# Performance work log

Measured on AMD Instinct MI355X. Metric: run time of the kernel, lower is better.

The kernel has to match this reference:

```python
import jax, jax.numpy as jnp
import numpy as np

N, K, D = 65536, 4096, 256
COMMITMENT_COST = 0.25


def setup_inputs() -> dict:
    key = jax.random.key(0)
    k1, k2 = jax.random.split(key)
    z_flat = jax.random.normal(k1, (N, D), dtype=jnp.float32)
    # init_method='normal': std=0.02
    codebook = jax.random.normal(k2, (K, D), dtype=jnp.float32) * 0.02
    return {"z_flat": z_flat, "codebook": codebook}


def reference(z_flat, codebook):
    # distances[n,k] = ||z_n||^2 + ||e_k||^2 - 2 z_n . e_k   (squared L2)
    z_sq = jnp.sum(z_flat ** 2, axis=1, keepdims=True)            # [N,1]
    e_sq = jnp.sum(codebook ** 2, axis=1)                          # [K]
    distances = z_sq + e_sq - 2.0 * jnp.matmul(z_flat, codebook.T)  # [N,K]
    indices = jnp.argmin(distances, axis=1)                        # [N] int
    quantized = codebook[indices]                                  # [N,D]

    e_latent_loss = jnp.mean((jax.lax.stop_gradient(quantized) - z_flat) ** 2)
    q_latent_loss = jnp.mean((quantized - jax.lax.stop_gradient(z_flat)) ** 2)
    loss = q_latent_loss + COMMITMENT_COST * e_latent_loss

    # straight-through estimator
    quantized_st = z_flat + jax.lax.stop_gradient(quantized - z_flat)
    return loss, quantized_st, indices
```

## Files before the change

kernel.cpp:

```cpp
#include <hip/hip_runtime.h>
#include <float.h>

typedef __attribute__((ext_vector_type(8))) short short8;
typedef __attribute__((ext_vector_type(16))) float f32x16;
typedef unsigned short u16;

#define N_ROWS 65536
#define K_CB   4096
#define D_DIM  256
#define TAU    1.0e-3f
#define RR     8

#define RB 128
#define KB 128
#define DB 32

#define WS_COUNTER 0
#define WS_ESQ     16
#define WS_IDX     (WS_ESQ + K_CB*4)
#define WS_FLAG    (WS_IDX + N_ROWS*4)
#define WS_PART    (WS_FLAG + N_ROWS*4)
#define NUM_OUT_BLOCKS ((N_ROWS*(D_DIM/4))/256)
#define WS_EH      (WS_PART + NUM_OUT_BLOCKS*8)
#define WS_EL      (WS_EH + K_CB*D_DIM*2)
#define WS_NEEDED  (WS_EL + (size_t)K_CB*D_DIM*2)

__device__ __forceinline__ u16 f2bf(float x) {
  unsigned int u = __float_as_uint(x);
  unsigned int r = (u + 0x7fffu + ((u >> 16) & 1u)) >> 16;
  return (u16)r;
}
__device__ __forceinline__ float bf2f(u16 b) {
  return __uint_as_float((unsigned int)b << 16);
}
__device__ __forceinline__ float np_score(float zsq, float ek, float dot) {
#pragma clang fp contract(off)
  float t1 = zsq + ek;
  float t2 = 2.0f * dot;
  return t1 - t2;
}

__device__ __forceinline__ float np_sum128_sq(const float* p) {
#pragma clang fp contract(off)
  float r0 = p[0]*p[0], r1 = p[1]*p[1], r2 = p[2]*p[2], r3 = p[3]*p[3];
  float r4 = p[4]*p[4], r5 = p[5]*p[5], r6 = p[6]*p[6], r7 = p[7]*p[7];
  for (int i = 8; i < 128; i += 8) {
    r0 += p[i+0]*p[i+0]; r1 += p[i+1]*p[i+1];
    r2 += p[i+2]*p[i+2]; r3 += p[i+3]*p[i+3];
    r4 += p[i+4]*p[i+4]; r5 += p[i+5]*p[i+5];
    r6 += p[i+6]*p[i+6]; r7 += p[i+7]*p[i+7];
  }
  return ((r0+r1)+(r2+r3))+((r4+r5)+(r6+r7));
}
__device__ __forceinline__ float np_sumsq256(const float* p) {
#pragma clang fp contract(off)
  float a = np_sum128_sq(p);
  float b = np_sum128_sq(p + 128);
  return a + b;
}

__global__ __launch_bounds__(256) void esq_np_kernel(const float* __restrict__ cb,
                                                     float* __restrict__ esq) {
  const int k = blockIdx.x * 256 + threadIdx.x;
  esq[k] = np_sumsq256(cb + (size_t)k * D_DIM);
}

__global__ __launch_bounds__(256) void esplit_perm_kernel(const float* __restrict__ cb,
                                                          u16* __restrict__ ehp,
                                                          u16* __restrict__ elp) {
  const int g  = blockIdx.x * 256 + threadIdx.x;
  const int k  = g >> 5;
  const int d8 = g & 31;
  const int kc = k >> 5, c = k & 31;
  const float* src = cb + (size_t)k * D_DIM + d8 * 8;
  float4 f0 = *(const float4*)src;
  float4 f1 = *(const float4*)(src + 4);
  float f[8] = {f0.x, f0.y, f0.z, f0.w, f1.x, f1.y, f1.z, f1.w};
  short8 h, lo;
  #pragma unroll
  for (int j = 0; j < 8; ++j) {
    u16 hb = f2bf(f[j]);
    h[j]  = (short)hb;
    lo[j] = (short)f2bf(f[j] - bf2f(hb));
  }
  const size_t off = (size_t)kc * 8192 + (size_t)d8 * 256 + (size_t)c * 8;
  *(short8*)(ehp + off) = h;
  *(short8*)(elp + off) = lo;
}

__global__ __launch_bounds__(256, 1) void mfma_argmin32_kernel(
    const float* __restrict__ z, const u16* __restrict__ ehp,
    const u16* __restrict__ elp, const float* __restrict__ esq,
    int* __restrict__ idx_out, int* __restrict__ flag,
    unsigned int* __restrict__ counter) {
  __shared__ u16 smem[2 * 16384];
  const int t   = threadIdx.x;
  const int w   = t >> 6;
  const int l   = t & 63;
  const int col = l & 31;
  const int hi  = l >> 5;
  const int rowbase = blockIdx.x * 256 + w * 64;
  const int wbase = w * 1024;

  short8 ah0[16], al0[16], ah1[16], al1[16];
  #pragma unroll
  for (int rb = 0; rb < 2; ++rb) {
    const float* zr = z + (size_t)(rowbase + rb * 32 + col) * D_DIM + hi * 8;
    #pragma unroll
    for (int s = 0; s < 16; ++s) {
      float4 f0 = *(const float4*)(zr + s * 16);
      float4 f1 = *(const float4*)(zr + s * 16 + 4);
      float f[8] = {f0.x, f0.y, f0.z, f0.w, f1.x, f1.y, f1.z, f1.w};
      short8 h, lo;
      #pragma unroll
      for (int j = 0; j < 8; ++j) {
        u16 hb = f2bf(f[j]);
        h[j]  = (short)hb;
        lo[j] = (short)f2bf(f[j] - bf2f(hb));
      }
      if (rb == 0) { ah0[s] = h; al0[s] = lo; }
      else         { ah1[s] = h; al1[s] = lo; }
    }
  }

  float m1[32], m2[32]; int ic[32];
  #pragma unroll
  for (int j = 0; j < 32; ++j) { m1[j] = FLT_MAX; m2[j] = FLT_MAX; ic[j] = 0; }

  #define STAGE(KCN, BUF) do {                                                  \
    char* lb = (char*)smem + (BUF) * 32768;                                     \
    const char* gh = (const char*)ehp + (size_t)(KCN) * 16384;                  \
    const char* gl = (const char*)elp + (size_t)(KCN) * 16384;                  \
    _Pragma("unroll")                                                           \
    for (int q = 0; q < 4; ++q) {                                               \
      __builtin_amdgcn_global_load_lds(                                         \
        (const __attribute__((address_space(1))) void*)(gh + q*4096 + t*16),    \
        (__attribute__((address_space(3))) void*)(lb + q*4096 + wbase),         \
        16, 0, 0);                                                              \
      __builtin_amdgcn_global_load_lds(                                         \
        (const __attribute__((address_space(1))) void*)(gl + q*4096 + t*16),    \
        (__attribute__((address_space(3))) void*)(lb + 16384 + q*4096 + wbase), \
        16, 0, 0);                                                              \
    }                                                                           \
  } while (0)

  STAGE(0, 0);
  __syncthreads();

  const int boff = hi * 512 + col * 16;
  for (int kc = 0; kc < 128; ++kc) {
    const int cur = kc & 1;
    if (kc + 1 < 128) STAGE(kc + 1, cur ^ 1);
    const char* bb = (const char*)smem + cur * 32768;

    f32x16 c0 = {}, c1 = {}, c2 = {}, c3 = {};
    #pragma unroll
    for (int s = 0; s < 16; ++s) {
      short8 bh = *(const short8*)(bb + s * 1024 + boff);
      short8 bl = *(const short8*)(bb + 16384 + s * 1024 + boff);
      c0 = __builtin_amdgcn_mfma_f32_32x32x16_bf16(ah0[s], bh, c0, 0, 0, 0);
      c1 = __builtin_amdgcn_mfma_f32_32x32x16_bf16(ah1[s], bh, c1, 0, 0, 0);
      c2 = __builtin_amdgcn_mfma_f32_32x32x16_bf16(al0[s], bh, c2, 0, 0, 0);
      c3 = __builtin_amdgcn_mfma_f32_32x32x16_bf16(al1[s], bh, c3, 0, 0, 0);
      c0 = __builtin_amdgcn_mfma_f32_32x32x16_bf16(ah0[s], bl, c0, 0, 0, 0);
      c1 = __builtin_amdgcn_mfma_f32_32x32x16_bf16(ah1[s], bl, c1, 0, 0, 0);
    }

    const float ev = esq[kc * 32 + col];
    #pragma unroll
    for (int r = 0; r < 16; ++r) {
      float sc0 = fmaf(-2.0f, c0[r] + c2[r], ev);
      bool lt0 = sc0 < m1[r];
      ic[r] = lt0 ? kc : ic[r];
      m2[r] = fminf(m2[r], fmaxf(m1[r], sc0));
      m1[r] = fminf(m1[r], sc0);
      float sc1 = fmaf(-2.0f, c1[r] + c3[r], ev);
      bool lt1 = sc1 < m1[16 + r];
      ic[16 + r] = lt1 ? kc : ic[16 + r];
      m2[16 + r] = fminf(m2[16 + r], fmaxf(m1[16 + r], sc1));
      m1[16 + r] = fminf(m1[16 + r], sc1);
    }
    __syncthreads();
  }
  #undef STAGE

  #pragma unroll
  for (int rb = 0; rb < 2; ++rb) {
    #pragma unroll
    for (int r = 0; r < 16; ++r) {
      const int j = rb * 16 + r;
      float a1 = m1[j], a2 = m2[j];
      int cd = ic[j] * 32 + col;
      #pragma unroll
      for (int off = 1; off < 32; off <<= 1) {
        float b1 = __shfl_xor(a1, off);
        float b2 = __shfl_xor(a2, off);
        int   bc = __shfl_xor(cd, off);
        bool take = (b1 < a1) || (b1 == a1 && bc < cd);
        float nm2 = take ? fminf(a1, b2) : fminf(a2, b1);
        if (take) { a1 = b1; cd = bc; }
        a2 = nm2;
      }
      if (col == 0) {
        const int orow = rowbase + rb * 32 + (r & 3) + 8 * (r >> 2) + 4 * hi;
        idx_out[orow] = cd;
        if (a2 - a1 < TAU) {
          unsigned int p = atomicAdd(counter, 1u);
          flag[p] = orow;
        }
      }
    }
  }
}

__global__ __launch_bounds__(256, 2) void argmin_kernel(
    const float4* __restrict__ z4, const float4* __restrict__ cb4,
    const float* __restrict__ esq, int* __restrict__ idx_out,
    int* __restrict__ flag, unsigned int* __restrict__ counter) {
  __shared__ float zt[DB][RB];
  __shared__ float et[DB][KB];
  const int t  = threadIdx.x;
  const int tr = t >> 4;
  const int tc = t & 15;
  const int row0 = blockIdx.x * RB;

  float min1[8], min2[8]; int idx1[8];
  #pragma unroll
  for (int i = 0; i < 8; ++i) { min1[i] = FLT_MAX; min2[i] = FLT_MAX; idx1[i] = 0; }

  for (int kc = 0; kc < K_CB / KB; ++kc) {
    const int k0 = kc * KB;
    float acc[8][8];
    #pragma unroll
    for (int i = 0; i < 8; ++i)
      #pragma unroll
      for (int j = 0; j < 8; ++j) acc[i][j] = 0.0f;

    float esqv[8];
    #pragma unroll
    for (int j = 0; j < 8; ++j) esqv[j] = esq[k0 + tc*8 + j];

    for (int dt = 0; dt < D_DIM / DB; ++dt) {
      __syncthreads();
      #pragma unroll
      for (int m = 0; m < 4; ++m) {
        int u  = t + 256*m;
        int dq = u & 7;
        int r  = u >> 3;
        float4 v = z4[(size_t)(row0 + r)*(D_DIM/4) + dt*8 + dq];
        zt[dq*4+0][r] = v.x; zt[dq*4+1][r] = v.y; zt[dq*4+2][r] = v.z; zt[dq*4+3][r] = v.w;
        float4 wv = cb4[(size_t)(k0 + r)*(D_DIM/4) + dt*8 + dq];
        et[dq*4+0][r] = wv.x; et[dq*4+1][r] = wv.y; et[dq*4+2][r] = wv.z; et[dq*4+3][r] = wv.w;
      }
      __syncthreads();

      #pragma unroll 8
      for (int d = 0; d < DB; ++d) {
        float4 za = *(const float4*)&zt[d][tr*8];
        float4 zb = *(const float4*)&zt[d][tr*8+4];
        float4 ea = *(const float4*)&et[d][tc*8];
        float4 eb = *(const float4*)&et[d][tc*8+4];
        float zr[8] = {za.x, za.y, za.z, za.w, zb.x, zb.y, zb.z, zb.w};
        float ev[8] = {ea.x, ea.y, ea.z, ea.w, eb.x, eb.y, eb.z, eb.w};
        #pragma unroll
        for (int i = 0; i < 8; ++i)
          #pragma unroll
          for (int j = 0; j < 8; ++j)
            acc[i][j] += zr[i] * ev[j];
      }
    }

    #pragma unroll
    for (int j = 0; j < 8; ++j) {
      const int k = k0 + tc*8 + j;
      #pragma unroll
      for (int i = 0; i < 8; ++i) {
        float s = esqv[j] - 2.0f * acc[i][j];
        if (s < min1[i]) { min2[i] = min1[i]; min1[i] = s; idx1[i] = k; }
        else if (s < min2[i]) { min2[i] = s; }
      }
    }
  }

  #pragma unroll
  for (int i = 0; i < 8; ++i) {
    float m1 = min1[i], m2 = min2[i]; int id = idx1[i];
    #pragma unroll
    for (int off = 1; off < 16; off <<= 1) {
      float om1 = __shfl_xor(m1, off);
      float om2 = __shfl_xor(m2, off);
      int   oid = __shfl_xor(id, off);
      bool take = (om1 < m1) || (om1 == m1 && oid < id);
      float nm2 = take ? fminf(m1, om2) : fminf(m2, om1);
      if (take) { m1 = om1; id = oid; }
      m2 = nm2;
    }
    if (tc == 0) {
      int row = row0 + tr*8 + i;
      idx_out[row] = id;
      if (m2 - m1 < TAU) {
        unsigned int p = atomicAdd(counter, 1u);
        flag[p] = row;
      }
    }
  }
}

__global__ __launch_bounds__(256) void refine_np_kernel(
    const float* __restrict__ z, const float* __restrict__ cb,
    const float* __restrict__ esq, int* __restrict__ idx_out,
    const int* __restrict__ flag, const unsigned int* __restrict__ counter) {
  __shared__ float zrow[RR][D_DIM];
  __shared__ float zsq[RR];
  __shared__ float rbest[256];
  __shared__ int   rbidx[256];
  const int t = threadIdx.x;
  const unsigned int cnt = *counter;
  const unsigned int ngroups = (cnt + RR - 1) / RR;

  for (unsigned int g = blockIdx.x; g < ngroups; g += gridDim.x) {
    __syncthreads();
    const int nr = (int)min((unsigned int)RR, cnt - g*RR);
    #pragma unroll
    for (int r = 0; r < RR; ++r) {
      int fi = (int)(g*RR) + ((r < nr) ? r : 0);
      int row = flag[fi];
      zrow[r][t] = z[(size_t)row * D_DIM + t];
    }
    __syncthreads();
    if (t < RR) zsq[t] = np_sumsq256(&zrow[t][0]);
    __syncthreads();

    float best[RR]; int bidx[RR];
    #pragma unroll
    for (int r = 0; r < RR; ++r) { best[r] = FLT_MAX; bidx[r] = 0x7fffffff; }

    for (int m = 0; m < K_CB / 256; ++m) {
      const int k = m*256 + t;
      const float4* e4 = (const float4*)(cb + (size_t)k * D_DIM);
      float acc[RR];
      #pragma unroll
      for (int r = 0; r < RR; ++r) acc[r] = 0.0f;
      for (int dq = 0; dq < D_DIM/4; ++dq) {
        float4 ev = e4[dq];
        #pragma unroll
        for (int r = 0; r < RR; ++r) {
          acc[r] = __fmaf_rn(zrow[r][dq*4+0], ev.x, acc[r]);
          acc[r] = __fmaf_rn(zrow[r][dq*4+1], ev.y, acc[r]);
          acc[r] = __fmaf_rn(zrow[r][dq*4+2], ev.z, acc[r]);
          acc[r] = __fmaf_rn(zrow[r][dq*4+3], ev.w, acc[r]);
        }
      }
      const float ek = esq[k];
      #pragma unroll
      for (int r = 0; r < RR; ++r) {
        float sc = np_score(zsq[r], ek, acc[r]);
        if (sc < best[r]) { best[r] = sc; bidx[r] = k; }
      }
    }

    for (int r = 0; r < RR; ++r) {
      __syncthreads();
      rbest[t] = best[r]; rbidx[t] = bidx[r];
      __syncthreads();
      for (int off = 128; off > 0; off >>= 1) {
        if (t < off) {
          float ob = rbest[t+off]; int oi = rbidx[t+off];
          if (ob < rbest[t] || (ob == rbest[t] && oi < rbidx[t])) {
            rbest[t] = ob; rbidx[t] = oi;
          }
        }
        __syncthreads();
      }
      if (t == 0 && r < nr) idx_out[flag[g*RR + r]] = rbidx[0];
    }
  }
}

__global__ __launch_bounds__(256) void output_kernel(
    const float4* __restrict__ z4, const float4* __restrict__ cb4,
    const int* __restrict__ idx_out, float* __restrict__ out,
    double* __restrict__ partials) {
  const int g  = blockIdx.x * 256 + threadIdx.x;
  const int n  = g >> 6;
  const int dq = g & 63;
  const int id = idx_out[n];
  float4 q  = cb4[(size_t)id * (D_DIM/4) + dq];
  float4 zv = z4[(size_t)n  * (D_DIM/4) + dq];
  float dx = q.x - zv.x, dy = q.y - zv.y, dz = q.z - zv.z, dw = q.w - zv.w;
  double psum = (double)dx*dx + (double)dy*dy + (double)dz*dz + (double)dw*dw;
  size_t base = 1 + (size_t)n * D_DIM + (size_t)dq * 4;
  out[base+0] = q.x; out[base+1] = q.y; out[base+2] = q.z; out[base+3] = q.w;
  if (dq == 0) out[1 + (size_t)N_ROWS*D_DIM + n] = (float)id;

  __shared__ double sred[256];
  sred[threadIdx.x] = psum;
  __syncthreads();
  for (int off = 128; off > 0; off >>= 1) {
    if (threadIdx.x < off) sred[threadIdx.x] += sred[threadIdx.x + off];
    __syncthreads();
  }
  if (threadIdx.x == 0) partials[blockIdx.x] = sred[0];
}

__global__ __launch_bounds__(256) void loss_kernel(const double* __restrict__ partials,
                                                   float* __restrict__ out) {
  const int t = threadIdx.x;
  double s = 0.0;
  for (int m = 0; m < NUM_OUT_BLOCKS/256; ++m) s += partials[t + 256*m];
  __shared__ double sred[256];
  sred[t] = s;
  __syncthreads();
  for (int off = 128; off > 0; off >>= 1) {
    if (t < off) sred[t] += sred[t + off];
    __syncthreads();
  }
  if (t == 0) out[0] = (float)(1.25 * sred[0] / ((double)N_ROWS * (double)D_DIM));
}

extern "C" void kernel_launch(void* const* d_in, const int* in_sizes, int n_in,
                              void* d_out, int out_size, void* d_ws, size_t ws_size,
                              hipStream_t stream) {
  const float* z  = (const float*)d_in[0];
  const float* cb = (const float*)d_in[1];
  float* out = (float*)d_out;
  char* ws = (char*)d_ws;

  unsigned int* counter = (unsigned int*)(ws + WS_COUNTER);
  float*  esq      = (float*) (ws + WS_ESQ);
  int*    idx      = (int*)   (ws + WS_IDX);
  int*    flag     = (int*)   (ws + WS_FLAG);
  double* partials = (double*)(ws + WS_PART);

  (void)hipMemsetAsync(ws, 0, 16, stream);
  esq_np_kernel<<<K_CB/256, 256, 0, stream>>>(cb, esq);

  if (ws_size >= WS_NEEDED) {
    u16* ehp = (u16*)(ws + WS_EH);
    u16* elp = (u16*)(ws + WS_EL);
    esplit_perm_kernel<<<(K_CB*(D_DIM/8))/256, 256, 0, stream>>>(cb, ehp, elp);
    mfma_argmin32_kernel<<<N_ROWS/256, 256, 0, stream>>>(z, ehp, elp, esq,
                                                         idx, flag, counter);
  } else {
    argmin_kernel<<<N_ROWS/RB, 256, 0, stream>>>((const float4*)z, (const float4*)cb,
                                                 esq, idx, flag, counter);
  }

  refine_np_kernel<<<256, 256, 0, stream>>>(z, cb, esq, idx, flag, counter);
  output_kernel<<<NUM_OUT_BLOCKS, 256, 0, stream>>>((const float4*)z, (const float4*)cb,
                                                    idx, out, partials);
  loss_kernel<<<1, 256, 0, stream>>>(partials, out);
}
```

Before: 621.6 us.

## Swap MFMA operand roles to 16x16x32 with codebook as A and z as B

Restructures the coarse argmin kernel to use 16x16x32 bf16 MFMAs, with codebook tiles in LDS as the A operand and z rows held in registers as B. Each wave now covers 32 rows instead of 64, with 128-row blocks and two blocks per CU, which shrinks per-thread argmin state from 32 rows to 2. The per-lane top-2 now runs within each lane over its codes, and the cross-lane reduction needs only two shuffle steps. The codebook permutation kernel writes a matching layout. The aim is higher occupancy and less register pressure and epilogue work, at the cost of loading each codebook tile from LDS for half as many rows per wave.

```diff
diff --git a/kernel.cpp b/kernel.cpp
--- a/kernel.cpp
+++ b/kernel.cpp
@@ -2,8 +2,9 @@
 #include <float.h>
 
 typedef __attribute__((ext_vector_type(8))) short short8;
-typedef __attribute__((ext_vector_type(16))) float f32x16;
+typedef __attribute__((ext_vector_type(4))) float f32x4;
 typedef unsigned short u16;
+typedef unsigned int u32;
 
 #define N_ROWS 65536
 #define K_CB   4096
@@ -65,17 +66,17 @@
   esq[k] = np_sumsq256(cb + (size_t)k * D_DIM);
 }
 
-__global__ __launch_bounds__(256) void esplit_perm_kernel(const float* __restrict__ cb,
-                                                          u16* __restrict__ ehp,
-                                                          u16* __restrict__ elp) {
+__global__ __launch_bounds__(256) void esplit_ca_kernel(const float* __restrict__ cb,
+                                                        u16* __restrict__ ehp,
+                                                        u16* __restrict__ elp) {
   const int g  = blockIdx.x * 256 + threadIdx.x;
-  const int k  = g >> 5;
-  const int d8 = g & 31;
-  const int kc = k >> 5, c = k & 31;
+  const int k  = g >> 5, d8 = g & 31;
+  const int c  = k >> 5, code = k & 31;
+  const int s  = d8 >> 2, lq = d8 & 3;
   const float* src = cb + (size_t)k * D_DIM + d8 * 8;
   float4 f0 = *(const float4*)src;
   float4 f1 = *(const float4*)(src + 4);
-  float f[8] = {f0.x, f0.y, f0.z, f0.w, f1.x, f1.y, f1.z, f1.w};
+  float f[8] = {f0.x,f0.y,f0.z,f0.w,f1.x,f1.y,f1.z,f1.w};
   short8 h, lo;
   #pragma unroll
   for (int j = 0; j < 8; ++j) {
@@ -83,34 +84,32 @@
     h[j]  = (short)hb;
     lo[j] = (short)f2bf(f[j] - bf2f(hb));
   }
-  const size_t off = (size_t)kc * 8192 + (size_t)d8 * 256 + (size_t)c * 8;
+  const size_t off = (size_t)c*8192 + s*1024 + lq*256 + code*8;
   *(short8*)(ehp + off) = h;
   *(short8*)(elp + off) = lo;
 }
 
-__global__ __launch_bounds__(256, 1) void mfma_argmin32_kernel(
+__global__ __launch_bounds__(256, 2) void coarse_ca_kernel(
     const float* __restrict__ z, const u16* __restrict__ ehp,
     const u16* __restrict__ elp, const float* __restrict__ esq,
     int* __restrict__ idx_out, int* __restrict__ flag,
-    unsigned int* __restrict__ counter) {
+    u32* __restrict__ counter) {
   __shared__ u16 smem[2 * 16384];
-  const int t   = threadIdx.x;
-  const int w   = t >> 6;
-  const int l   = t & 63;
-  const int col = l & 31;
-  const int hi  = l >> 5;
-  const int rowbase = blockIdx.x * 256 + w * 64;
+  const int t = threadIdx.x;
+  const int w = t >> 6, l = t & 63;
+  const int l16 = l & 15, lq = l >> 4;
+  const int rowbase = blockIdx.x * 128 + w * 32;
   const int wbase = w * 1024;
 
-  short8 ah0[16], al0[16], ah1[16], al1[16];
+  short8 bzh[2][8], bzl[2][8];
   #pragma unroll
-  for (int rb = 0; rb < 2; ++rb) {
-    const float* zr = z + (size_t)(rowbase + rb * 32 + col) * D_DIM + hi * 8;
-    #pragma unroll
-    for (int s = 0; s < 16; ++s) {
-      float4 f0 = *(const float4*)(zr + s * 16);
-      float4 f1 = *(const float4*)(zr + s * 16 + 4);
-      float f[8] = {f0.x, f0.y, f0.z, f0.w, f1.x, f1.y, f1.z, f1.w};
+  for (int rs = 0; rs < 2; ++rs) {
+    const float* zp = z + (size_t)(rowbase + rs*16 + l16) * D_DIM + lq*8;
+    #pragma unroll
+    for (int s = 0; s < 8; ++s) {
+      float4 f0 = *(const float4*)(zp + s*32);
+      float4 f1 = *(const float4*)(zp + s*32 + 4);
+      float f[8] = {f0.x,f0.y,f0.z,f0.w,f1.x,f1.y,f1.z,f1.w};
       short8 h, lo;
       #pragma unroll
       for (int j = 0; j < 8; ++j) {
@@ -118,14 +117,13 @@
         h[j]  = (short)hb;
         lo[j] = (short)f2bf(f[j] - bf2f(hb));
       }
-      if (rb == 0) { ah0[s] = h; al0[s] = lo; }
-      else         { ah1[s] = h; al1[s] = lo; }
-    }
-  }
-
-  float m1[32], m2[32]; int ic[32];
-  #pragma unroll
-  for (int j = 0; j < 32; ++j) { m1[j] = FLT_MAX; m2[j] = FLT_MAX; ic[j] = 0; }
+      bzh[rs][s] = h; bzl[rs][s] = lo;
+    }
+  }
+
+  float m1[2] = {FLT_MAX, FLT_MAX};
+  float m2[2] = {FLT_MAX, FLT_MAX};
+  int   ic[2] = {0, 0};
 
   #define STAGE(KCN, BUF) do {                                                  \
     char* lb = (char*)smem + (BUF) * 32768;                                     \
@@ -147,67 +145,86 @@
   STAGE(0, 0);
   __syncthreads();
 
-  const int boff = hi * 512 + col * 16;
-  for (int kc = 0; kc < 128; ++kc) {
-    const int cur = kc & 1;
-    if (kc + 1 < 128) STAGE(kc + 1, cur ^ 1);
+  #define MFMA16(A, B, C) __builtin_amdgcn_mfma_f32_16x16x32_bf16(A, B, C, 0, 0, 0)
+  #define TOP2(RS, SC, CODE) do {                                               \
+    bool lt_ = (SC) < m1[RS];                                                   \
+    m2[RS] = fminf(m2[RS], fmaxf(m1[RS], (SC)));                                \
+    ic[RS] = lt_ ? (CODE) : ic[RS];                                             \
+    m1[RS] = fminf(m1[RS], (SC));                                               \
+  } while (0)
+
+  for (int cc = 0; cc < 128; ++cc) {
+    const int cur = cc & 1;
+    if (cc + 1 < 128) STAGE(cc + 1, cur ^ 1);
     const char* bb = (const char*)smem + cur * 32768;
-
-    f32x16 c0 = {}, c1 = {}, c2 = {}, c3 = {};
-    #pragma unroll
-    for (int s = 0; s < 16; ++s) {
-      short8 bh = *(const short8*)(bb + s * 1024 + boff);
-      short8 bl = *(const short8*)(bb + 16384 + s * 1024 + boff);
-      c0 = __builtin_amdgcn_mfma_f32_32x32x16_bf16(ah0[s], bh, c0, 0, 0, 0);
-      c1 = __builtin_amdgcn_mfma_f32_32x32x16_bf16(ah1[s], bh, c1, 0, 0, 0);
-      c2 = __builtin_amdgcn_mfma_f32_32x32x16_bf16(al0[s], bh, c2, 0, 0, 0);
-      c3 = __builtin_amdgcn_mfma_f32_32x32x16_bf16(al1[s], bh, c3, 0, 0, 0);
-      c0 = __builtin_amdgcn_mfma_f32_32x32x16_bf16(ah0[s], bl, c0, 0, 0, 0);
-      c1 = __builtin_amdgcn_mfma_f32_32x32x16_bf16(ah1[s], bl, c1, 0, 0, 0);
-    }
-
-    const float ev = esq[kc * 32 + col];
-    #pragma unroll
-    for (int r = 0; r < 16; ++r) {
-      float sc0 = fmaf(-2.0f, c0[r] + c2[r], ev);
-      bool lt0 = sc0 < m1[r];
-      ic[r] = lt0 ? kc : ic[r];
-      m2[r] = fminf(m2[r], fmaxf(m1[r], sc0));
-      m1[r] = fminf(m1[r], sc0);
-      float sc1 = fmaf(-2.0f, c1[r] + c3[r], ev);
-      bool lt1 = sc1 < m1[16 + r];
-      ic[16 + r] = lt1 ? kc : ic[16 + r];
-      m2[16 + r] = fminf(m2[16 + r], fmaxf(m1[16 + r], sc1));
-      m1[16 + r] = fminf(m1[16 + r], sc1);
+    float4 e0 = *(const float4*)(esq + cc*32 + lq*4);
+    float4 e1 = *(const float4*)(esq + cc*32 + 16 + lq*4);
+
+    f32x4 a00 = {}, a01 = {}, a10 = {}, a11 = {};
+    #pragma unroll
+    for (int s = 0; s < 8; ++s) {
+      const int ao = s*2048 + lq*512 + l16*16;
+      short8 ah0 = *(const short8*)(bb + ao);
+      short8 ah1 = *(const short8*)(bb + ao + 256);
+      short8 al0 = *(const short8*)(bb + 16384 + ao);
+      short8 al1 = *(const short8*)(bb + 16384 + ao + 256);
+      a00 = MFMA16(ah0, bzh[0][s], a00);
+      a01 = MFMA16(ah0, bzh[1][s], a01);
+      a10 = MFMA16(ah1, bzh[0][s], a10);
+      a11 = MFMA16(ah1, bzh[1][s], a11);
+      a00 = MFMA16(ah0, bzl[0][s], a00);
+      a01 = MFMA16(ah0, bzl[1][s], a01);
+      a10 = MFMA16(ah1, bzl[0][s], a10);
+      a11 = MFMA16(ah1, bzl[1][s], a11);
+      a00 = MFMA16(al0, bzh[0][s], a00);
+      a01 = MFMA16(al0, bzh[1][s], a01);
+      a10 = MFMA16(al1, bzh[0][s], a10);
+      a11 = MFMA16(al1, bzh[1][s], a11);
+    }
+
+    #pragma unroll
+    for (int r = 0; r < 4; ++r) {
+      const float ev = ((const float*)&e0)[r];
+      const int code = cc*32 + lq*4 + r;
+      float s0 = fmaf(-2.0f, a00[r], ev);
+      TOP2(0, s0, code);
+      float s1 = fmaf(-2.0f, a01[r], ev);
+      TOP2(1, s1, code);
+    }
+    #pragma unroll
+    for (int r = 0; r < 4; ++r) {
+      const float ev = ((const float*)&e1)[r];
+      const int code = cc*32 + 16 + lq*4 + r;
+      float s0 = fmaf(-2.0f, a10[r], ev);
+      TOP2(0, s0, code);
+      float s1 = fmaf(-2.0f, a11[r], ev);
+      TOP2(1, s1, code);
     }
     __syncthreads();
   }
   #undef STAGE
+  #undef MFMA16
+  #undef TOP2
 
   #pragma unroll
-  for (int rb = 0; rb < 2; ++rb) {
-    #pragma unroll
-    for (int r = 0; r < 16; ++r) {
-      const int j = rb * 16 + r;
-      float a1 = m1[j], a2 = m2[j];
-      int cd = ic[j] * 32 + col;
-      #pragma unroll
-      for (int off = 1; off < 32; off <<= 1) {
-        float b1 = __shfl_xor(a1, off);
-        float b2 = __shfl_xor(a2, off);
-        int   bc = __shfl_xor(cd, off);
-        bool take = (b1 < a1) || (b1 == a1 && bc < cd);
-        float nm2 = take ? fminf(a1, b2) : fminf(a2, b1);
-        if (take) { a1 = b1; cd = bc; }
-        a2 = nm2;
-      }
-      if (col == 0) {
-        const int orow = rowbase + rb * 32 + (r & 3) + 8 * (r >> 2) + 4 * hi;
-        idx_out[orow] = cd;
-        if (a2 - a1 < TAU) {
-          unsigned int p = atomicAdd(counter, 1u);
-          flag[p] = orow;
-        }
+  for (int rs = 0; rs < 2; ++rs) {
+    float a1 = m1[rs], a2 = m2[rs]; int cd = ic[rs];
+    #pragma unroll
+    for (int off = 16; off < 64; off <<= 1) {
+      float b1 = __shfl_xor(a1, off);
+      float b2 = __shfl_xor(a2, off);
+      int   bc = __shfl_xor(cd, off);
+      bool take = (b1 < a1) || (b1 == a1 && bc < cd);
+      float nm2 = take ? fminf(a1, b2) : fminf(a2, b1);
+      if (take) { a1 = b1; cd = bc; }
+      a2 = nm2;
+    }
+    if (lq == 0) {
+      const int row = rowbase + rs*16 + l16;
+      idx_out[row] = cd;
+      if (a2 - a1 < TAU) {
+        u32 p = atomicAdd(counter, 1u);
+        flag[p] = row;
       }
     }
   }
@@ -438,9 +455,9 @@
   if (ws_size >= WS_NEEDED) {
     u16* ehp = (u16*)(ws + WS_EH);
     u16* elp = (u16*)(ws + WS_EL);
-    esplit_perm_kernel<<<(K_CB*(D_DIM/8))/256, 256, 0, stream>>>(cb, ehp, elp);
-    mfma_argmin32_kernel<<<N_ROWS/256, 256, 0, stream>>>(z, ehp, elp, esq,
-                                                         idx, flag, counter);
+    esplit_ca_kernel<<<(K_CB*(D_DIM/8))/256, 256, 0, stream>>>(cb, ehp, elp);
+    coarse_ca_kernel<<<N_ROWS/128, 256, 0, stream>>>(z, ehp, elp, esq,
+                                                     idx, flag, counter);
   } else {
     argmin_kernel<<<N_ROWS/RB, 256, 0, stream>>>((const float4*)z, (const float4*)cb,
                                                  esq, idx, flag, counter);
```

Result: faster. 538.3 us (-13.4%).
